# Performance work log

Hardware: AMD Instinct MI355X
Metric: run time of the kernel (lower is better)

## Reference

```python
import jax, jax.numpy as jnp
import numpy as np

B, N, D = 8, 4096, 512

def setup_inputs() -> dict:
    key = jax.random.key(0)
    k1, k2, k3 = jax.random.split(key, 3)
    x = jax.random.normal(k1, (B, N, D), dtype=jnp.float32)
    rotation = jax.random.normal(k2, (D, D), dtype=jnp.float32)
    entangle = jax.random.normal(k3, (D, D), dtype=jnp.float32)
    return {"x": x, "rotation": rotation, "entangle": entangle}

def reference(x, rotation, entangle):
    # query/key projections; note: no V projection, V = x
    query = jnp.einsum("bnd,de->bne", x, rotation)
    key = jnp.einsum("bnd,de->bne", x, entangle)
    scale = 1.0 / jnp.sqrt(jnp.asarray(x.shape[-1], dtype=x.dtype))
    scores = jax.nn.softmax(jnp.einsum("bqd,bkd->bqk", query, key) * scale, axis=-1)
    return jnp.einsum("bqk,bkd->bqd", scores, x)
```

## Files before the change

kernel.cpp:

```cpp
#include <hip/hip_runtime.h>

#define BATCH 8
#define SEQ   4096
#define DIM   512

typedef __attribute__((ext_vector_type(8))) short bf16x8;
typedef __attribute__((ext_vector_type(4))) float f32x4;

__device__ __forceinline__ unsigned short f2bf(float f) {
  unsigned int u = __float_as_uint(f);
  unsigned int r = (u + 0x7fffu + ((u >> 16) & 1u)) >> 16;
  return (unsigned short)r;
}
__device__ __forceinline__ float bf2f(unsigned short s) {
  return __uint_as_float(((unsigned int)s) << 16);
}

__device__ __forceinline__ void gload_lds16(const void* g, void* l) {
  __builtin_amdgcn_global_load_lds(
      (const __attribute__((address_space(1))) unsigned int*)g,
      (__attribute__((address_space(3))) unsigned int*)l, 16, 0, 0);
}

__global__ __launch_bounds__(256) void wt_split_kernel(
    const float* __restrict__ rot, const float* __restrict__ ent,
    unsigned short* __restrict__ wrh, unsigned short* __restrict__ wrl,
    unsigned short* __restrict__ weh, unsigned short* __restrict__ wel) {
  const float scale = 0.04419417382415922f;
  int g = blockIdx.x * 256 + threadIdx.x;
  for (int idx = g; idx < 512 * 512; idx += 128 * 256) {
    int d = idx >> 9, e = idx & 511;
    size_t o = (size_t)e * 512 + d;
    float v = rot[idx] * scale;
    unsigned short h = f2bf(v);
    wrh[o] = h; wrl[o] = f2bf(v - bf2f(h));
    float v2 = ent[idx];
    unsigned short h2 = f2bf(v2);
    weh[o] = h2; wel[o] = f2bf(v2 - bf2f(h2));
  }
}

__global__ __launch_bounds__(256) void xt_split_kernel(
    const float* __restrict__ X, unsigned short* __restrict__ Th,
    unsigned short* __restrict__ Xh, unsigned short* __restrict__ Xl) {
  __shared__ float T[64][65];
  const int b = blockIdx.z, n0 = blockIdx.x * 64, d0 = blockIdx.y * 64;
  const int tid = threadIdx.x;
  for (int idx = tid; idx < 4096; idx += 256) {
    int r = idx >> 6, c = idx & 63;
    size_t gi = ((size_t)(b * SEQ + n0 + r)) * DIM + d0 + c;
    float v = X[gi];
    T[r][c] = v;
    unsigned short h = f2bf(v);
    Xh[gi] = h;
    Xl[gi] = f2bf(v - bf2f(h));
  }
  __syncthreads();
  for (int idx = tid; idx < 4096; idx += 256) {
    int r = idx >> 6, c = idx & 63;
    size_t o = ((size_t)(b * DIM + d0 + r)) * SEQ + n0 + c;
    Th[o] = f2bf(T[c][r]);
  }
}

__global__ __launch_bounds__(256, 2) void proj_both(
    const unsigned short* __restrict__ Xh, const unsigned short* __restrict__ Xl,
    const unsigned short* __restrict__ wrh, const unsigned short* __restrict__ wrl,
    const unsigned short* __restrict__ weh, const unsigned short* __restrict__ wel,
    unsigned short* __restrict__ qh, unsigned short* __restrict__ ql,
    unsigned short* __restrict__ kh, unsigned short* __restrict__ kl) {
  const int tid = threadIdx.x;
  const int w = tid >> 6, lane = tid & 63, l15 = lane & 15, quad = lane >> 4;
  const int rowBase = blockIdx.x * 64 + (w & 1) * 32;
  const int colBase = blockIdx.y * 64 + (w >> 1) * 32;
  f32x4 qa[2][2] = {}, ka[2][2] = {};
  const unsigned short *xph[2], *xpl[2];
  const unsigned short *rh[2], *rl[2], *eh[2], *el[2];
#pragma unroll
  for (int mi = 0; mi < 2; ++mi) {
    size_t o = (size_t)(rowBase + mi * 16 + l15) * DIM + quad * 8;
    xph[mi] = Xh + o; xpl[mi] = Xl + o;
  }
#pragma unroll
  for (int ni = 0; ni < 2; ++ni) {
    size_t o = (size_t)(colBase + ni * 16 + l15) * DIM + quad * 8;
    rh[ni] = wrh + o; rl[ni] = wrl + o; eh[ni] = weh + o; el[ni] = wel + o;
  }
  for (int d0 = 0; d0 < DIM; d0 += 32) {
    bf16x8 ah[2], al[2];
#pragma unroll
    for (int mi = 0; mi < 2; ++mi) {
      ah[mi] = *(const bf16x8*)(xph[mi] + d0);
      al[mi] = *(const bf16x8*)(xpl[mi] + d0);
    }
#pragma unroll
    for (int ni = 0; ni < 2; ++ni) {
      bf16x8 bh = *(const bf16x8*)(rh[ni] + d0);
      bf16x8 bl = *(const bf16x8*)(rl[ni] + d0);
      bf16x8 ch = *(const bf16x8*)(eh[ni] + d0);
      bf16x8 cl = *(const bf16x8*)(el[ni] + d0);
#pragma unroll
      for (int mi = 0; mi < 2; ++mi) {
        qa[mi][ni] = __builtin_amdgcn_mfma_f32_16x16x32_bf16(ah[mi], bh, qa[mi][ni], 0, 0, 0);
        qa[mi][ni] = __builtin_amdgcn_mfma_f32_16x16x32_bf16(ah[mi], bl, qa[mi][ni], 0, 0, 0);
        qa[mi][ni] = __builtin_amdgcn_mfma_f32_16x16x32_bf16(al[mi], bh, qa[mi][ni], 0, 0, 0);
        ka[mi][ni] = __builtin_amdgcn_mfma_f32_16x16x32_bf16(ah[mi], ch, ka[mi][ni], 0, 0, 0);
        ka[mi][ni] = __builtin_amdgcn_mfma_f32_16x16x32_bf16(ah[mi], cl, ka[mi][ni], 0, 0, 0);
        ka[mi][ni] = __builtin_amdgcn_mfma_f32_16x16x32_bf16(al[mi], ch, ka[mi][ni], 0, 0, 0);
      }
    }
  }
#pragma unroll
  for (int mi = 0; mi < 2; ++mi)
#pragma unroll
    for (int ni = 0; ni < 2; ++ni)
#pragma unroll
      for (int r = 0; r < 4; ++r) {
        int row = rowBase + mi * 16 + quad * 4 + r;
        int col = colBase + ni * 16 + l15;
        size_t o = (size_t)row * DIM + col;
        float v = qa[mi][ni][r];
        unsigned short h = f2bf(v);
        qh[o] = h; ql[o] = f2bf(v - bf2f(h));
        float v2 = ka[mi][ni][r];
        unsigned short h2 = f2bf(v2);
        kh[o] = h2; kl[o] = f2bf(v2 - bf2f(h2));
      }
}

__global__ __launch_bounds__(256, 2) void attn_mfma(
    const unsigned short* __restrict__ Qh, const unsigned short* __restrict__ Ql,
    const unsigned short* __restrict__ Kh, const unsigned short* __restrict__ Kl,
    const unsigned short* __restrict__ Xth, float* __restrict__ out,
    float* __restrict__ Opart, float* __restrict__ Mp, float* __restrict__ Lp) {
  __shared__ short stage[2][8192];
  __shared__ float red1[32][2], red2[32][2], al_s[32], l_s[32];
  unsigned short* const PsH = (unsigned short*)&stage[1][0];

  const int tid = threadIdx.x;
  const int w = tid >> 6, lane = tid & 63, l15 = lane & 15, quad = lane >> 4;
  const int wq = w & 1, wk = w >> 1;
  const int b = blockIdx.x, q0 = blockIdx.y * 32;
  const int iters = (SEQ / 128) / gridDim.z;
  const int kbase = blockIdx.z * iters * 128;
  const int dbase = w * 128;

  const size_t qoff = (size_t)(b * SEQ + q0 + wq * 16 + l15) * DIM + quad * 8;
  const unsigned short* qph = Qh + qoff;
  const unsigned short* qpl = Ql + qoff;

  const int r0 = tid >> 2;
  const int clog = (tid & 3) ^ (r0 & 3);
  const unsigned short* kpl[2] = {Kh + (size_t)b * SEQ * DIM,
                                  Kl + (size_t)b * SEQ * DIM};
  auto STAGE = [&](int bsel, int krow, int cc) {
#pragma unroll
    for (int j = 0; j < 4; ++j) {
      const int row = (j & 1) * 64 + r0;
      gload_lds16(kpl[j >> 1] + (size_t)(krow + row) * DIM + cc * 32 + clog * 8,
                  &stage[bsel][j * 2048 + w * 512]);
    }
  };

  f32x4 Of[2][8] = {};
  float m_r[4], l_r[4];
#pragma unroll
  for (int r = 0; r < 4; ++r) { m_r[r] = -3.0e38f; l_r[r] = 0.0f; }

  STAGE(0, kbase, 0);
  __syncthreads();

  for (int t = 0; t < iters; ++t) {
    const int k0 = kbase + t * 128;
    f32x4 sa[4] = {};

#pragma unroll
    for (int c = 0; c < 16; ++c) {
      if (c < 15) STAGE((c + 1) & 1, k0, c + 1);
      else if (t + 1 < iters) STAGE(0, k0 + 128, 0);
      bf16x8 ah = *(const bf16x8*)(qph + c * 32);
      bf16x8 al = *(const bf16x8*)(qpl + c * 32);
      const short* bufp = &stage[c & 1][0];
      const int cq = (quad ^ (l15 & 3)) * 8;
#pragma unroll
      for (int s = 0; s < 4; ++s) {
        const int kr = wk * 64 + s * 16 + l15;
        bf16x8 bh = *(const bf16x8*)(bufp + kr * 32 + cq);
        bf16x8 bl = *(const bf16x8*)(bufp + 4096 + kr * 32 + cq);
        sa[s] = __builtin_amdgcn_mfma_f32_16x16x32_bf16(ah, bh, sa[s], 0, 0, 0);
        sa[s] = __builtin_amdgcn_mfma_f32_16x16x32_bf16(ah, bl, sa[s], 0, 0, 0);
        sa[s] = __builtin_amdgcn_mfma_f32_16x16x32_bf16(al, bh, sa[s], 0, 0, 0);
      }
      __syncthreads();
    }

    float pm[4];
#pragma unroll
    for (int r = 0; r < 4; ++r) {
      float v = fmaxf(fmaxf(sa[0][r], sa[1][r]), fmaxf(sa[2][r], sa[3][r]));
#pragma unroll
      for (int off = 1; off < 16; off <<= 1) v = fmaxf(v, __shfl_xor(v, off, 64));
      pm[r] = v;
    }
    if (l15 == 0) {
#pragma unroll
      for (int r = 0; r < 4; ++r) red1[wq * 16 + quad * 4 + r][wk] = pm[r];
    }
    __syncthreads();
    float al_r[4];
#pragma unroll
    for (int r = 0; r < 4; ++r) {
      const int row = wq * 16 + quad * 4 + r;
      float mn = fmaxf(m_r[r], fmaxf(red1[row][0], red1[row][1]));
      al_r[r] = __expf(m_r[r] - mn);
      m_r[r] = mn;
    }
#pragma unroll
    for (int r = 0; r < 4; ++r) {
      const int row = wq * 16 + quad * 4 + r, rx = row & 15;
      float sum = 0.0f;
#pragma unroll
      for (int s = 0; s < 4; ++s) {
        float p = __expf(sa[s][r] - m_r[r]);
        sum += p;
        const int col = wk * 64 + s * 16 + l15;
        PsH[row * 128 + ((col >> 3) ^ rx) * 8 + (col & 7)] = f2bf(p);
      }
#pragma unroll
      for (int off = 1; off < 16; off <<= 1) sum += __shfl_xor(sum, off, 64);
      if (l15 == 0) {
        red2[row][wk] = sum;
        if (wk == 0) al_s[row] = al_r[r];
      }
    }
    __syncthreads();
#pragma unroll
    for (int r = 0; r < 4; ++r) {
      const int row = wq * 16 + quad * 4 + r;
      l_r[r] = l_r[r] * al_r[r] + red2[row][0] + red2[row][1];
    }

    float alv[2][4];
#pragma unroll
    for (int qt = 0; qt < 2; ++qt)
#pragma unroll
      for (int r = 0; r < 4; ++r) alv[qt][r] = al_s[qt * 16 + quad * 4 + r];
#pragma unroll
    for (int qt = 0; qt < 2; ++qt)
#pragma unroll
      for (int nt = 0; nt < 8; ++nt)
#pragma unroll
        for (int r = 0; r < 4; ++r) Of[qt][nt][r] *= alv[qt][r];

    const unsigned short* Xb =
        Xth + ((size_t)(b * DIM + dbase) + l15) * SEQ + k0 + quad * 8;
#pragma unroll
    for (int ks = 0; ks < 4; ++ks) {
      bf16x8 Ph[2];
#pragma unroll
      for (int qt = 0; qt < 2; ++qt) {
        const int prow = qt * 16 + l15;
        const int sb = (ks * 4 + quad) ^ l15;
        Ph[qt] = *(const bf16x8*)(PsH + prow * 128 + sb * 8);
      }
#pragma unroll
      for (int nh = 0; nh < 2; ++nh) {
        bf16x8 xf[4];
#pragma unroll
        for (int i = 0; i < 4; ++i)
          xf[i] = *(const bf16x8*)(Xb + (size_t)((nh * 4 + i) * 16) * SEQ + ks * 32);
#pragma unroll
        for (int i = 0; i < 4; ++i)
#pragma unroll
          for (int qt = 0; qt < 2; ++qt)
            Of[qt][nh * 4 + i] = __builtin_amdgcn_mfma_f32_16x16x32_bf16(
                Ph[qt], xf[i], Of[qt][nh * 4 + i], 0, 0, 0);
      }
    }
    __syncthreads();
  }

  if (wk == 0 && l15 == 0) {
#pragma unroll
    for (int r = 0; r < 4; ++r) l_s[wq * 16 + quad * 4 + r] = l_r[r];
    if (gridDim.z > 1) {
      size_t ri = (size_t)blockIdx.z * (BATCH * SEQ) + (size_t)b * SEQ + q0 +
                  wq * 16 + quad * 4;
#pragma unroll
      for (int r = 0; r < 4; ++r) { Mp[ri + r] = m_r[r]; Lp[ri + r] = l_r[r]; }
    }
  }
  __syncthreads();

  if (gridDim.z == 1) {
    float inv[2][4];
#pragma unroll
    for (int qt = 0; qt < 2; ++qt)
#pragma unroll
      for (int r = 0; r < 4; ++r) inv[qt][r] = 1.0f / l_s[qt * 16 + quad * 4 + r];
#pragma unroll
    for (int qt = 0; qt < 2; ++qt)
#pragma unroll
      for (int r = 0; r < 4; ++r) {
        const size_t ro =
            ((size_t)(b * SEQ + q0 + qt * 16 + quad * 4 + r)) * DIM + dbase;
#pragma unroll
        for (int nt = 0; nt < 8; ++nt)
          out[ro + nt * 16 + l15] = Of[qt][nt][r] * inv[qt][r];
      }
  } else {
    float* Ob = (blockIdx.z == 0) ? out : Opart;
#pragma unroll
    for (int qt = 0; qt < 2; ++qt)
#pragma unroll
      for (int r = 0; r < 4; ++r) {
        const size_t ro =
            ((size_t)(b * SEQ + q0 + qt * 16 + quad * 4 + r)) * DIM + dbase;
#pragma unroll
        for (int nt = 0; nt < 8; ++nt) Ob[ro + nt * 16 + l15] = Of[qt][nt][r];
      }
  }
}

__global__ __launch_bounds__(256) void merge_kernel(
    float* __restrict__ out, const float* __restrict__ Op,
    const float* __restrict__ Mp, const float* __restrict__ Lp) {
  const int NR = BATCH * SEQ;
  size_t e = ((size_t)blockIdx.x * 256 + threadIdx.x) * 4;
  int row = (int)(e >> 9);
  float m0 = Mp[row], m1 = Mp[NR + row];
  float l0 = Lp[row], l1 = Lp[NR + row];
  float m = fmaxf(m0, m1);
  float a0 = __expf(m0 - m), a1 = __expf(m1 - m);
  float inv = 1.0f / (a0 * l0 + a1 * l1);
  float4 o0 = *(const float4*)(out + e);
  float4 o1 = *(const float4*)(Op + e);
  float4 r;
  r.x = (a0 * o0.x + a1 * o1.x) * inv;
  r.y = (a0 * o0.y + a1 * o1.y) * inv;
  r.z = (a0 * o0.z + a1 * o1.z) * inv;
  r.w = (a0 * o0.w + a1 * o1.w) * inv;
  *(float4*)(out + e) = r;
}

extern "C" void kernel_launch(void* const* d_in, const int* in_sizes, int n_in,
                              void* d_out, int out_size, void* d_ws,
                              size_t ws_size, hipStream_t stream) {
  const float* x   = (const float*)d_in[0];
  const float* rot = (const float*)d_in[1];
  const float* ent = (const float*)d_in[2];
  float* out = (float*)d_out;

  const size_t NE = (size_t)BATCH * SEQ * DIM;
  unsigned short* qh  = (unsigned short*)d_ws;
  unsigned short* ql  = qh + NE;
  unsigned short* kh  = ql + NE;
  unsigned short* kl  = kh + NE;
  unsigned short* xth = kl + NE;
  unsigned short* xh  = xth + NE;
  unsigned short* xl  = xh + NE;
  unsigned short* wrh = xl + NE;
  unsigned short* wrl = wrh + 262144;
  unsigned short* weh = wrl + 262144;
  unsigned short* wel = weh + 262144;
  float* Opart = (float*)(wel + 262144);
  float* Mp    = Opart + NE;
  float* Lp    = Mp + 2 * (BATCH * SEQ);

  const size_t need2 =
      (7 * NE + 4 * 262144) * sizeof(unsigned short) +
      (NE + 4 * (size_t)(BATCH * SEQ)) * sizeof(float);
  const int splits = (ws_size >= need2) ? 2 : 1;

  wt_split_kernel<<<128, 256, 0, stream>>>(rot, ent, wrh, wrl, weh, wel);
  xt_split_kernel<<<dim3(SEQ / 64, DIM / 64, BATCH), 256, 0, stream>>>(x, xth, xh, xl);
  proj_both<<<dim3(BATCH * SEQ / 64, DIM / 64), 256, 0, stream>>>(
      xh, xl, wrh, wrl, weh, wel, qh, ql, kh, kl);

  attn_mfma<<<dim3(BATCH, SEQ / 32, splits), 256, 0, stream>>>(
      qh, ql, kh, kl, xth, out, Opart, Mp, Lp);
  if (splits == 2) {
    merge_kernel<<<(unsigned)(NE / 1024), 256, 0, stream>>>(out, Opart, Mp, Lp);
  }
}
```

Baseline: 1.745 ms.

## Triple-buffer K/Q staging ring with explicit waitcnt barriers and MFMA priority

Replaces the double-buffered K staging with a 3-slot LDS ring that prefetches two chunks ahead. Q hi/lo tiles now also go through LDS via async global-to-LDS loads instead of direct global reads. Each __syncthreads becomes a partial vmcnt/lgkmcnt wait plus s_barrier, which keeps loads in flight across the barrier, and MFMA sections are wrapped in s_setprio. PsH moves to its own LDS buffer, so LDS use rises, and the hand-counted vmcnt(5) depends on the exact number of loads issued per stage.

```diff
diff --git a/kernel.cpp b/kernel.cpp
--- a/kernel.cpp
+++ b/kernel.cpp
@@ -133,33 +133,37 @@
     const unsigned short* __restrict__ Kh, const unsigned short* __restrict__ Kl,
     const unsigned short* __restrict__ Xth, float* __restrict__ out,
     float* __restrict__ Opart, float* __restrict__ Mp, float* __restrict__ Lp) {
-  __shared__ short stage[2][8192];
+  __shared__ short ring[3][10240];
+  __shared__ unsigned short PsH[32 * 128];
   __shared__ float red1[32][2], red2[32][2], al_s[32], l_s[32];
-  unsigned short* const PsH = (unsigned short*)&stage[1][0];
 
   const int tid = threadIdx.x;
   const int w = tid >> 6, lane = tid & 63, l15 = lane & 15, quad = lane >> 4;
   const int wq = w & 1, wk = w >> 1;
   const int b = blockIdx.x, q0 = blockIdx.y * 32;
   const int iters = (SEQ / 128) / gridDim.z;
+  const int NC = iters * 16;
   const int kbase = blockIdx.z * iters * 128;
   const int dbase = w * 128;
 
-  const size_t qoff = (size_t)(b * SEQ + q0 + wq * 16 + l15) * DIM + quad * 8;
-  const unsigned short* qph = Qh + qoff;
-  const unsigned short* qpl = Ql + qoff;
-
   const int r0 = tid >> 2;
-  const int clog = (tid & 3) ^ (r0 & 3);
-  const unsigned short* kpl[2] = {Kh + (size_t)b * SEQ * DIM,
-                                  Kl + (size_t)b * SEQ * DIM};
-  auto STAGE = [&](int bsel, int krow, int cc) {
+  const int clogK = (tid & 3) ^ (r0 & 3);
+  const unsigned short* kplane[2] = {Kh + (size_t)b * SEQ * DIM,
+                                     Kl + (size_t)b * SEQ * DIM};
+  const int qrow = (tid >> 2) & 31;
+  const int clogQ = (tid & 3) ^ (qrow & 3);
+  const unsigned short* qsrc =
+      ((tid >> 7) ? Ql : Qh) + (size_t)(b * SEQ + q0 + qrow) * DIM + clogQ * 8;
+
+  auto STAGE = [&](int slot, int krow0, int cc) {
+    short* base = &ring[slot][0];
 #pragma unroll
     for (int j = 0; j < 4; ++j) {
-      const int row = (j & 1) * 64 + r0;
-      gload_lds16(kpl[j >> 1] + (size_t)(krow + row) * DIM + cc * 32 + clog * 8,
-                  &stage[bsel][j * 2048 + w * 512]);
-    }
+      gload_lds16(
+          kplane[j >> 1] + (size_t)(krow0 + (j & 1) * 64 + r0) * DIM + cc * 32 + clogK * 8,
+          base + j * 2048 + w * 512);
+    }
+    gload_lds16(qsrc + cc * 32, base + 8192 + w * 512);
   };
 
   f32x4 Of[2][8] = {};
@@ -168,30 +172,45 @@
   for (int r = 0; r < 4; ++r) { m_r[r] = -3.0e38f; l_r[r] = 0.0f; }
 
   STAGE(0, kbase, 0);
-  __syncthreads();
-
+  STAGE(1, kbase, 1);
+
+  int sl = 0;
   for (int t = 0; t < iters; ++t) {
     const int k0 = kbase + t * 128;
     f32x4 sa[4] = {};
 
 #pragma unroll
     for (int c = 0; c < 16; ++c) {
-      if (c < 15) STAGE((c + 1) & 1, k0, c + 1);
-      else if (t + 1 < iters) STAGE(0, k0 + 128, 0);
-      bf16x8 ah = *(const bf16x8*)(qph + c * 32);
-      bf16x8 al = *(const bf16x8*)(qpl + c * 32);
-      const short* bufp = &stage[c & 1][0];
+      if (t == iters - 1 && c == 15) {
+        asm volatile("s_waitcnt vmcnt(0)" ::: "memory");
+      } else {
+        asm volatile("s_waitcnt vmcnt(5)" ::: "memory");
+      }
+      __builtin_amdgcn_sched_barrier(0);
+      __builtin_amdgcn_s_barrier();
+      {
+        const int gn = t * 16 + c + 2;
+        if (gn < NC) {
+          int slot2 = sl + 2; if (slot2 >= 3) slot2 -= 3;
+          STAGE(slot2, kbase + (gn >> 4) * 128, gn & 15);
+        }
+      }
+      const short* base = &ring[sl][0];
       const int cq = (quad ^ (l15 & 3)) * 8;
+      bf16x8 ah = *(const bf16x8*)(base + 8192 + (wq * 16 + l15) * 32 + cq);
+      bf16x8 al = *(const bf16x8*)(base + 9216 + (wq * 16 + l15) * 32 + cq);
+      __builtin_amdgcn_s_setprio(1);
 #pragma unroll
       for (int s = 0; s < 4; ++s) {
         const int kr = wk * 64 + s * 16 + l15;
-        bf16x8 bh = *(const bf16x8*)(bufp + kr * 32 + cq);
-        bf16x8 bl = *(const bf16x8*)(bufp + 4096 + kr * 32 + cq);
+        bf16x8 bh = *(const bf16x8*)(base + kr * 32 + cq);
+        bf16x8 bl = *(const bf16x8*)(base + 4096 + kr * 32 + cq);
         sa[s] = __builtin_amdgcn_mfma_f32_16x16x32_bf16(ah, bh, sa[s], 0, 0, 0);
         sa[s] = __builtin_amdgcn_mfma_f32_16x16x32_bf16(ah, bl, sa[s], 0, 0, 0);
         sa[s] = __builtin_amdgcn_mfma_f32_16x16x32_bf16(al, bh, sa[s], 0, 0, 0);
       }
-      __syncthreads();
+      __builtin_amdgcn_s_setprio(0);
+      sl = (sl + 1 == 3) ? 0 : sl + 1;
     }
 
     float pm[4];
@@ -206,7 +225,9 @@
 #pragma unroll
       for (int r = 0; r < 4; ++r) red1[wq * 16 + quad * 4 + r][wk] = pm[r];
     }
-    __syncthreads();
+    asm volatile("s_waitcnt lgkmcnt(0)" ::: "memory");
+    __builtin_amdgcn_sched_barrier(0);
+    __builtin_amdgcn_s_barrier();
     float al_r[4];
 #pragma unroll
     for (int r = 0; r < 4; ++r) {
@@ -233,7 +254,9 @@
         if (wk == 0) al_s[row] = al_r[r];
       }
     }
-    __syncthreads();
+    asm volatile("s_waitcnt lgkmcnt(0)" ::: "memory");
+    __builtin_amdgcn_sched_barrier(0);
+    __builtin_amdgcn_s_barrier();
 #pragma unroll
     for (int r = 0; r < 4; ++r) {
       const int row = wq * 16 + quad * 4 + r;
@@ -269,15 +292,16 @@
 #pragma unroll
         for (int i = 0; i < 4; ++i)
           xf[i] = *(const bf16x8*)(Xb + (size_t)((nh * 4 + i) * 16) * SEQ + ks * 32);
+        __builtin_amdgcn_s_setprio(1);
 #pragma unroll
         for (int i = 0; i < 4; ++i)
 #pragma unroll
           for (int qt = 0; qt < 2; ++qt)
             Of[qt][nh * 4 + i] = __builtin_amdgcn_mfma_f32_16x16x32_bf16(
                 Ph[qt], xf[i], Of[qt][nh * 4 + i], 0, 0, 0);
-      }
-    }
-    __syncthreads();
+        __builtin_amdgcn_s_setprio(0);
+      }
+    }
   }
 
   if (wk == 0 && l15 == 0) {
```

Result: no change. 1.714 ms (-1.8%).

## Restructure attention kernel: 8 waves, Q pinned in LDS, K tiles in registers

Applied to the files above, without the earlier changes.

Rewrites the attention kernel to run 512 threads (8 waves) per block over 256-key tiles. The Q hi/lo block is pinned in LDS once per block, and K fragments are loaded straight from global memory into double-buffered registers, replacing the LDS K staging and its per-chunk barriers. Softmax reductions now run across 8 waves, with explicit waitcnt plus barrier, and each wave owns 64 output dims. It also adds s_setprio around the MFMA bursts. The aim is to remove the 16 per-tile syncthreads and the LDS staging traffic, at the cost of higher register pressure and uncoalesced-ish direct K reads.

```diff
diff --git a/kernel.cpp b/kernel.cpp
--- a/kernel.cpp
+++ b/kernel.cpp
@@ -128,185 +128,182 @@
       }
 }
 
-__global__ __launch_bounds__(256, 2) void attn_mfma(
+#define LOADK(BUF, KROW0, CC)                                                  \
+  do {                                                                         \
+    _Pragma("unroll") for (int s_ = 0; s_ < 2; ++s_) {                         \
+      const size_t ro_ =                                                       \
+          (size_t)((KROW0) + w * 32 + s_ * 16 + l15) * DIM + (CC)*32 + quad * 8; \
+      kb[BUF][s_][0] = *(const bf16x8*)(kpl0 + ro_);                           \
+      kb[BUF][s_][1] = *(const bf16x8*)(kpl1 + ro_);                           \
+    }                                                                          \
+  } while (0)
+
+__global__ __launch_bounds__(512, 2) void attn_mfma(
     const unsigned short* __restrict__ Qh, const unsigned short* __restrict__ Ql,
     const unsigned short* __restrict__ Kh, const unsigned short* __restrict__ Kl,
     const unsigned short* __restrict__ Xth, float* __restrict__ out,
     float* __restrict__ Opart, float* __restrict__ Mp, float* __restrict__ Lp) {
-  __shared__ short stage[2][8192];
-  __shared__ float red1[32][2], red2[32][2], al_s[32], l_s[32];
-  unsigned short* const PsH = (unsigned short*)&stage[1][0];
+  __shared__ short Qpin[32768];
+  __shared__ unsigned short PsH[8192];
+  __shared__ float red1[32][8], red2[32][8];
 
   const int tid = threadIdx.x;
   const int w = tid >> 6, lane = tid & 63, l15 = lane & 15, quad = lane >> 4;
-  const int wq = w & 1, wk = w >> 1;
   const int b = blockIdx.x, q0 = blockIdx.y * 32;
-  const int iters = (SEQ / 128) / gridDim.z;
-  const int kbase = blockIdx.z * iters * 128;
-  const int dbase = w * 128;
-
-  const size_t qoff = (size_t)(b * SEQ + q0 + wq * 16 + l15) * DIM + quad * 8;
-  const unsigned short* qph = Qh + qoff;
-  const unsigned short* qpl = Ql + qoff;
-
-  const int r0 = tid >> 2;
-  const int clog = (tid & 3) ^ (r0 & 3);
-  const unsigned short* kpl[2] = {Kh + (size_t)b * SEQ * DIM,
-                                  Kl + (size_t)b * SEQ * DIM};
-  auto STAGE = [&](int bsel, int krow, int cc) {
-#pragma unroll
-    for (int j = 0; j < 4; ++j) {
-      const int row = (j & 1) * 64 + r0;
-      gload_lds16(kpl[j >> 1] + (size_t)(krow + row) * DIM + cc * 32 + clog * 8,
-                  &stage[bsel][j * 2048 + w * 512]);
-    }
-  };
-
-  f32x4 Of[2][8] = {};
-  float m_r[4], l_r[4];
-#pragma unroll
-  for (int r = 0; r < 4; ++r) { m_r[r] = -3.0e38f; l_r[r] = 0.0f; }
-
-  STAGE(0, kbase, 0);
+  const int iters = (SEQ / 256) / gridDim.z;
+  const int kbase = blockIdx.z * iters * 256;
+  const int dbase = w * 64;
+
+#pragma unroll
+  for (int j = 0; j < 8; ++j) {
+    const int row = (j & 3) * 8 + w;
+    const unsigned short* src =
+        ((j >> 2) ? Ql : Qh) + (size_t)(b * SEQ + q0 + row) * DIM + (lane ^ w) * 8;
+    gload_lds16(src, &Qpin[j * 4096 + w * 512]);
+  }
   __syncthreads();
 
+  const unsigned short* kpl0 = Kh + (size_t)b * SEQ * DIM;
+  const unsigned short* kpl1 = Kl + (size_t)b * SEQ * DIM;
+
+  bf16x8 kb[2][2][2];
+  f32x4 Of[2][4] = {};
+  float m_r[2][4], l_r[2][4];
+#pragma unroll
+  for (int qs = 0; qs < 2; ++qs)
+#pragma unroll
+    for (int r = 0; r < 4; ++r) { m_r[qs][r] = -3.0e38f; l_r[qs][r] = 0.0f; }
+
+  LOADK(0, kbase, 0);
+
   for (int t = 0; t < iters; ++t) {
-    const int k0 = kbase + t * 128;
-    f32x4 sa[4] = {};
+    const int k0 = kbase + t * 256;
+    f32x4 sa[2][2] = {};
 
 #pragma unroll
     for (int c = 0; c < 16; ++c) {
-      if (c < 15) STAGE((c + 1) & 1, k0, c + 1);
-      else if (t + 1 < iters) STAGE(0, k0 + 128, 0);
-      bf16x8 ah = *(const bf16x8*)(qph + c * 32);
-      bf16x8 al = *(const bf16x8*)(qpl + c * 32);
-      const short* bufp = &stage[c & 1][0];
-      const int cq = (quad ^ (l15 & 3)) * 8;
-#pragma unroll
-      for (int s = 0; s < 4; ++s) {
-        const int kr = wk * 64 + s * 16 + l15;
-        bf16x8 bh = *(const bf16x8*)(bufp + kr * 32 + cq);
-        bf16x8 bl = *(const bf16x8*)(bufp + 4096 + kr * 32 + cq);
-        sa[s] = __builtin_amdgcn_mfma_f32_16x16x32_bf16(ah, bh, sa[s], 0, 0, 0);
-        sa[s] = __builtin_amdgcn_mfma_f32_16x16x32_bf16(ah, bl, sa[s], 0, 0, 0);
-        sa[s] = __builtin_amdgcn_mfma_f32_16x16x32_bf16(al, bh, sa[s], 0, 0, 0);
-      }
-      __syncthreads();
-    }
-
-    float pm[4];
-#pragma unroll
-    for (int r = 0; r < 4; ++r) {
-      float v = fmaxf(fmaxf(sa[0][r], sa[1][r]), fmaxf(sa[2][r], sa[3][r]));
-#pragma unroll
-      for (int off = 1; off < 16; off <<= 1) v = fmaxf(v, __shfl_xor(v, off, 64));
-      pm[r] = v;
-    }
-    if (l15 == 0) {
-#pragma unroll
-      for (int r = 0; r < 4; ++r) red1[wq * 16 + quad * 4 + r][wk] = pm[r];
-    }
-    __syncthreads();
-    float al_r[4];
-#pragma unroll
-    for (int r = 0; r < 4; ++r) {
-      const int row = wq * 16 + quad * 4 + r;
-      float mn = fmaxf(m_r[r], fmaxf(red1[row][0], red1[row][1]));
-      al_r[r] = __expf(m_r[r] - mn);
-      m_r[r] = mn;
-    }
-#pragma unroll
-    for (int r = 0; r < 4; ++r) {
-      const int row = wq * 16 + quad * 4 + r, rx = row & 15;
-      float sum = 0.0f;
-#pragma unroll
-      for (int s = 0; s < 4; ++s) {
-        float p = __expf(sa[s][r] - m_r[r]);
-        sum += p;
-        const int col = wk * 64 + s * 16 + l15;
-        PsH[row * 128 + ((col >> 3) ^ rx) * 8 + (col & 7)] = f2bf(p);
-      }
-#pragma unroll
-      for (int off = 1; off < 16; off <<= 1) sum += __shfl_xor(sum, off, 64);
-      if (l15 == 0) {
-        red2[row][wk] = sum;
-        if (wk == 0) al_s[row] = al_r[r];
-      }
-    }
-    __syncthreads();
-#pragma unroll
-    for (int r = 0; r < 4; ++r) {
-      const int row = wq * 16 + quad * 4 + r;
-      l_r[r] = l_r[r] * al_r[r] + red2[row][0] + red2[row][1];
-    }
-
-    float alv[2][4];
+      if (c < 15) {
+        LOADK((c + 1) & 1, k0, c + 1);
+      } else if (t + 1 < iters) {
+        LOADK(0, k0 + 256, 0);
+      }
+      bf16x8 qfh[2], qfl[2];
+#pragma unroll
+      for (int qs = 0; qs < 2; ++qs) {
+        const int row = qs * 16 + l15;
+        const int off = row * 512 + ((c * 4 + quad) ^ (l15 & 7)) * 8;
+        qfh[qs] = *(const bf16x8*)&Qpin[off];
+        qfl[qs] = *(const bf16x8*)&Qpin[16384 + off];
+      }
+      __builtin_amdgcn_s_setprio(1);
+#pragma unroll
+      for (int qs = 0; qs < 2; ++qs)
+#pragma unroll
+        for (int s = 0; s < 2; ++s) {
+          sa[qs][s] = __builtin_amdgcn_mfma_f32_16x16x32_bf16(
+              qfh[qs], kb[c & 1][s][0], sa[qs][s], 0, 0, 0);
+          sa[qs][s] = __builtin_amdgcn_mfma_f32_16x16x32_bf16(
+              qfh[qs], kb[c & 1][s][1], sa[qs][s], 0, 0, 0);
+          sa[qs][s] = __builtin_amdgcn_mfma_f32_16x16x32_bf16(
+              qfl[qs], kb[c & 1][s][0], sa[qs][s], 0, 0, 0);
+        }
+      __builtin_amdgcn_s_setprio(0);
+    }
+
+#pragma unroll
+    for (int qs = 0; qs < 2; ++qs)
+#pragma unroll
+      for (int r = 0; r < 4; ++r) {
+        float v = fmaxf(sa[qs][0][r], sa[qs][1][r]);
+#pragma unroll
+        for (int off = 1; off < 16; off <<= 1) v = fmaxf(v, __shfl_xor(v, off, 64));
+        if (l15 == 0) red1[qs * 16 + quad * 4 + r][w] = v;
+      }
+    asm volatile("s_waitcnt lgkmcnt(0)" ::: "memory");
+    __builtin_amdgcn_sched_barrier(0);
+    __builtin_amdgcn_s_barrier();
+
+    float al_r[2][4];
+#pragma unroll
+    for (int qs = 0; qs < 2; ++qs)
+#pragma unroll
+      for (int r = 0; r < 4; ++r) {
+        const int row = qs * 16 + quad * 4 + r;
+        f32x4 ra = *(const f32x4*)&red1[row][0];
+        f32x4 rb = *(const f32x4*)&red1[row][4];
+        float mx = fmaxf(fmaxf(fmaxf(ra[0], ra[1]), fmaxf(ra[2], ra[3])),
+                         fmaxf(fmaxf(rb[0], rb[1]), fmaxf(rb[2], rb[3])));
+        float mn = fmaxf(m_r[qs][r], mx);
+        al_r[qs][r] = __expf(m_r[qs][r] - mn);
+        m_r[qs][r] = mn;
+        float p0 = __expf(sa[qs][0][r] - mn);
+        float p1 = __expf(sa[qs][1][r] - mn);
+        const int c0 = w * 32 + l15, c1 = c0 + 16;
+        PsH[row * 256 + ((c0 >> 3) ^ row) * 8 + (c0 & 7)] = f2bf(p0);
+        PsH[row * 256 + ((c1 >> 3) ^ row) * 8 + (c1 & 7)] = f2bf(p1);
+        float sum = p0 + p1;
+#pragma unroll
+        for (int off = 1; off < 16; off <<= 1) sum += __shfl_xor(sum, off, 64);
+        if (l15 == 0) red2[row][w] = sum;
+      }
+    asm volatile("s_waitcnt lgkmcnt(0)" ::: "memory");
+    __builtin_amdgcn_sched_barrier(0);
+    __builtin_amdgcn_s_barrier();
+
+#pragma unroll
+    for (int qs = 0; qs < 2; ++qs)
+#pragma unroll
+      for (int r = 0; r < 4; ++r) {
+        const int row = qs * 16 + quad * 4 + r;
+        f32x4 ra = *(const f32x4*)&red2[row][0];
+        f32x4 rb = *(const f32x4*)&red2[row][4];
+        l_r[qs][r] = l_r[qs][r] * al_r[qs][r] +
+                     (ra[0] + ra[1] + ra[2] + ra[3] + rb[0] + rb[1] + rb[2] + rb[3]);
+      }
+
 #pragma unroll
     for (int qt = 0; qt < 2; ++qt)
 #pragma unroll
-      for (int r = 0; r < 4; ++r) alv[qt][r] = al_s[qt * 16 + quad * 4 + r];
-#pragma unroll
-    for (int qt = 0; qt < 2; ++qt)
-#pragma unroll
-      for (int nt = 0; nt < 8; ++nt)
-#pragma unroll
-        for (int r = 0; r < 4; ++r) Of[qt][nt][r] *= alv[qt][r];
+      for (int nt = 0; nt < 4; ++nt)
+#pragma unroll
+        for (int r = 0; r < 4; ++r) Of[qt][nt][r] *= al_r[qt][r];
 
     const unsigned short* Xb =
         Xth + ((size_t)(b * DIM + dbase) + l15) * SEQ + k0 + quad * 8;
 #pragma unroll
-    for (int ks = 0; ks < 4; ++ks) {
+    for (int ks = 0; ks < 8; ++ks) {
       bf16x8 Ph[2];
 #pragma unroll
       for (int qt = 0; qt < 2; ++qt) {
         const int prow = qt * 16 + l15;
-        const int sb = (ks * 4 + quad) ^ l15;
-        Ph[qt] = *(const bf16x8*)(PsH + prow * 128 + sb * 8);
-      }
-#pragma unroll
-      for (int nh = 0; nh < 2; ++nh) {
-        bf16x8 xf[4];
-#pragma unroll
-        for (int i = 0; i < 4; ++i)
-          xf[i] = *(const bf16x8*)(Xb + (size_t)((nh * 4 + i) * 16) * SEQ + ks * 32);
-#pragma unroll
-        for (int i = 0; i < 4; ++i)
-#pragma unroll
-          for (int qt = 0; qt < 2; ++qt)
-            Of[qt][nh * 4 + i] = __builtin_amdgcn_mfma_f32_16x16x32_bf16(
-                Ph[qt], xf[i], Of[qt][nh * 4 + i], 0, 0, 0);
-      }
-    }
-    __syncthreads();
-  }
-
-  if (wk == 0 && l15 == 0) {
-#pragma unroll
-    for (int r = 0; r < 4; ++r) l_s[wq * 16 + quad * 4 + r] = l_r[r];
-    if (gridDim.z > 1) {
-      size_t ri = (size_t)blockIdx.z * (BATCH * SEQ) + (size_t)b * SEQ + q0 +
-                  wq * 16 + quad * 4;
-#pragma unroll
-      for (int r = 0; r < 4; ++r) { Mp[ri + r] = m_r[r]; Lp[ri + r] = l_r[r]; }
-    }
-  }
-  __syncthreads();
+        const int phys = (ks * 4 + quad) ^ prow;
+        Ph[qt] = *(const bf16x8*)&PsH[prow * 256 + phys * 8];
+      }
+      bf16x8 xf[4];
+#pragma unroll
+      for (int i = 0; i < 4; ++i)
+        xf[i] = *(const bf16x8*)(Xb + (size_t)(i * 16) * SEQ + ks * 32);
+      __builtin_amdgcn_s_setprio(1);
+#pragma unroll
+      for (int i = 0; i < 4; ++i)
+#pragma unroll
+        for (int qt = 0; qt < 2; ++qt)
+          Of[qt][i] = __builtin_amdgcn_mfma_f32_16x16x32_bf16(
+              Ph[qt], xf[i], Of[qt][i], 0, 0, 0);
+      __builtin_amdgcn_s_setprio(0);
+    }
+  }
 
   if (gridDim.z == 1) {
-    float inv[2][4];
 #pragma unroll
     for (int qt = 0; qt < 2; ++qt)
 #pragma unroll
-      for (int r = 0; r < 4; ++r) inv[qt][r] = 1.0f / l_s[qt * 16 + quad * 4 + r];
-#pragma unroll
-    for (int qt = 0; qt < 2; ++qt)
-#pragma unroll
-      for (int r = 0; r < 4; ++r) {
+      for (int r = 0; r < 4; ++r) {
+        const float inv = 1.0f / l_r[qt][r];
         const size_t ro =
             ((size_t)(b * SEQ + q0 + qt * 16 + quad * 4 + r)) * DIM + dbase;
 #pragma unroll
-        for (int nt = 0; nt < 8; ++nt)
-          out[ro + nt * 16 + l15] = Of[qt][nt][r] * inv[qt][r];
+        for (int i = 0; i < 4; ++i) out[ro + i * 16 + l15] = Of[qt][i][r] * inv;
       }
   } else {
     float* Ob = (blockIdx.z == 0) ? out : Opart;
@@ -317,8 +314,18 @@
         const size_t ro =
             ((size_t)(b * SEQ + q0 + qt * 16 + quad * 4 + r)) * DIM + dbase;
 #pragma unroll
-        for (int nt = 0; nt < 8; ++nt) Ob[ro + nt * 16 + l15] = Of[qt][nt][r];
-      }
+        for (int i = 0; i < 4; ++i) Ob[ro + i * 16 + l15] = Of[qt][i][r];
+      }
+    if (w == 0 && l15 == 0) {
+      size_t ri = (size_t)blockIdx.z * (BATCH * SEQ) + (size_t)b * SEQ + q0;
+#pragma unroll
+      for (int qs = 0; qs < 2; ++qs)
+#pragma unroll
+        for (int r = 0; r < 4; ++r) {
+          Mp[ri + qs * 16 + quad * 4 + r] = m_r[qs][r];
+          Lp[ri + qs * 16 + quad * 4 + r] = l_r[qs][r];
+        }
+    }
   }
 }
 
@@ -377,7 +384,7 @@
   proj_both<<<dim3(BATCH * SEQ / 64, DIM / 64), 256, 0, stream>>>(
       xh, xl, wrh, wrl, weh, wel, qh, ql, kh, kl);
 
-  attn_mfma<<<dim3(BATCH, SEQ / 32, splits), 256, 0, stream>>>(
+  attn_mfma<<<dim3(BATCH, SEQ / 32, splits), 512, 0, stream>>>(
       qh, ql, kh, kl, xth, out, Opart, Mp, Lp);
   if (splits == 2) {
     merge_kernel<<<(unsigned)(NE / 1024), 256, 0, stream>>>(out, Opart, Mp, Lp);
```

After: 2.057 ms. 1.18x slower.
